# Optimization experiments

Hardware: AMD Instinct MI355X
Metric: run time of the kernel (lower is better)

## Reference

```python
import jax, jax.numpy as jnp
import numpy as np

B, T, D = 64, 512, 512
H, DH = 8, 64  # head_num, att_embedding_size; H*DH == D
NEG = jnp.float32(-2.0**32 + 1)


def _pos_encoding(t, d):
    # Position_Embedding (mode='sum'): [cos, sin] concat over d/2 frequencies
    inv_freq = 1.0 / jnp.power(10000.0, 2.0 * jnp.arange(d // 2, dtype=jnp.float32) / d)
    pij = jnp.arange(t, dtype=jnp.float32)[:, None] * inv_freq[None, :]  # (T, d/2)
    return jnp.concatenate([jnp.cos(pij), jnp.sin(pij)], axis=-1)  # (T, d)


def setup_inputs() -> dict:
    key = jax.random.key(0)
    ks = jax.random.split(key, 9)
    queries = jax.random.normal(ks[0], (B, T, D), dtype=jnp.float32)
    keys = jax.random.normal(ks[1], (B, T, D), dtype=jnp.float32)
    query_lens = jax.random.randint(ks[2], (B, 1), 1, T + 1)
    key_lens = jax.random.randint(ks[3], (B, 1), 1, T + 1)
    W_Q = jax.random.truncated_normal(ks[4], -2., 2., (D, H * DH), dtype=jnp.float32) * 0.05
    W_K = jax.random.truncated_normal(ks[5], -2., 2., (D, H * DH), dtype=jnp.float32) * 0.05
    W_V = jax.random.truncated_normal(ks[6], -2., 2., (D, H * DH), dtype=jnp.float32) * 0.05
    fw1 = jax.random.normal(ks[7], (H * DH, 4 * H * DH), dtype=jnp.float32) * 0.02
    fw2 = jax.random.normal(ks[8], (4 * H * DH, H * DH), dtype=jnp.float32) * 0.02
    return {"queries": queries, "keys": keys, "query_lens": query_lens,
            "key_lens": key_lens, "W_Q": W_Q, "W_K": W_K, "W_V": W_V,
            "fw1": fw1, "fw2": fw2}


def reference(queries, keys, query_lens, key_lens, W_Q, W_K, W_V, fw1, fw2):
    # sequence masks (B, T) from lengths (B, 1)
    ar = jnp.arange(T)
    q_mask = (ar[None, :] < query_lens).astype(jnp.float32)  # (B, T)
    k_mask = ar[None, :] < key_lens                          # (B, T) bool

    pe = _pos_encoding(T, D)[None]  # (1, T, D)
    q_in = queries + pe
    k_in = keys + pe

    qp = jnp.einsum('btd,de->bte', q_in, W_Q).reshape(B, T, H, DH)
    kp = jnp.einsum('btd,de->bte', k_in, W_K)
    # DeepCTR quirk: values projected from the already-projected keys
    vp = jnp.einsum('btd,de->bte', kp, W_V).reshape(B, T, H, DH)
    kp = kp.reshape(B, T, H, DH)

    scores = jnp.einsum('bthd,bshd->bhts', qp, kp) / jnp.sqrt(jnp.float32(DH))
    scores = jnp.where(k_mask[:, None, None, :], scores, NEG)
    scores = scores - jnp.max(scores, axis=-1, keepdims=True)
    attn = jax.nn.softmax(scores, axis=-1)
    attn = attn * q_mask[:, None, :, None]

    out = jnp.einsum('bhts,bshd->bthd', attn, vp).reshape(B, T, H * DH)
    result = out + q_in  # residual uses PE-augmented queries

    ff = jnp.einsum('btd,df->btf', jax.nn.relu(jnp.einsum('btd,df->btf', result, fw1)), fw2)
    result = result + ff

    return jnp.mean(result, axis=1, keepdims=True)  # (B, 1, D)
```

## Files before the change

### kernel.cpp

```cpp
#include <hip/hip_runtime.h>

typedef unsigned short u16;
typedef __attribute__((ext_vector_type(8))) short short8;
typedef __attribute__((ext_vector_type(4))) float floatx4;

#define QSCALE 0.1803368801111204f

__device__ __forceinline__ u16 f2bf(float x) {
  union { float f; unsigned u; } un; un.f = x;
  unsigned r = un.u + 0x7fffu + ((un.u >> 16) & 1u);
  return (u16)(r >> 16);
}
__device__ __forceinline__ float bf2f(u16 h) {
  union { unsigned u; float f; } un; un.u = ((unsigned)h) << 16;
  return un.f;
}
__device__ __forceinline__ void gld16(const u16* g, u16* l) {
  __builtin_amdgcn_global_load_lds((__attribute__((address_space(1))) void*)g,
                                   (__attribute__((address_space(3))) void*)l, 16, 0, 0);
}

__global__ __launch_bounds__(256) void wtrans_all(const float* __restrict__ W_Q,
                                                  const float* __restrict__ W_K,
                                                  const float* __restrict__ fw1,
                                                  u16* __restrict__ WqT, u16* __restrict__ WkT,
                                                  u16* __restrict__ F1T) {
  __shared__ float tile[32][33];
  int L = blockIdx.x;
  const float* in;
  u16* out;
  int N, bx, by;
  if (L < 256) { in = W_Q; out = WqT; N = 512; bx = L & 15; by = L >> 4; }
  else if (L < 512) { L -= 256; in = W_K; out = WkT; N = 512; bx = L & 15; by = L >> 4; }
  else { L -= 512; in = fw1; out = F1T; N = 2048; bx = L & 63; by = L >> 6; }
  int tx = threadIdx.x, ty = threadIdx.y;
  int n0 = bx * 32, k0 = by * 32;
#pragma unroll
  for (int i = 0; i < 4; i++) {
    int kk = ty + i * 8;
    tile[kk][tx] = in[(size_t)(k0 + kk) * N + n0 + tx];
  }
  __syncthreads();
#pragma unroll
  for (int i = 0; i < 4; i++) {
    int nn = ty + i * 8;
    out[(size_t)(n0 + nn) * 512 + k0 + tx] = f2bf(tile[tx][nn]);
  }
}

__global__ __launch_bounds__(256) void wkv_kernel(const float* __restrict__ WK,
                                                  const float* __restrict__ WV,
                                                  u16* __restrict__ WkvT) {
  __shared__ float Kt[32][36];
  __shared__ float Vt[32][36];
  int nt = blockIdx.x & 15, dt = blockIdx.x >> 4;
  int n0 = nt * 32, d0 = dt * 32;
  int tid = threadIdx.x;
  int flat = tid * 4;
  int i4 = flat >> 5, j4 = flat & 31;
  int tn = tid & 15, td = tid >> 4;
  float acc00 = 0.f, acc01 = 0.f, acc10 = 0.f, acc11 = 0.f;
  for (int e0 = 0; e0 < 512; e0 += 32) {
    __syncthreads();
    *(float4*)&Kt[i4][j4] = *(const float4*)&WK[(size_t)(d0 + i4) * 512 + e0 + j4];
    *(float4*)&Vt[i4][j4] = *(const float4*)&WV[(size_t)(e0 + i4) * 512 + n0 + j4];
    __syncthreads();
#pragma unroll 8
    for (int e = 0; e < 32; e++) {
      float k0v = Kt[td * 2][e], k1v = Kt[td * 2 + 1][e];
      float v0 = Vt[e][tn * 2], v1 = Vt[e][tn * 2 + 1];
      acc00 += k0v * v0; acc01 += k0v * v1;
      acc10 += k1v * v0; acc11 += k1v * v1;
    }
  }
  size_t o = (size_t)(n0 + tn * 2) * 512 + d0 + td * 2;
  WkvT[o] = f2bf(acc00);
  WkvT[o + 1] = f2bf(acc10);
  WkvT[o + 512] = f2bf(acc01);
  WkvT[o + 513] = f2bf(acc11);
}

__global__ __launch_bounds__(256) void pe_add_kernel(const float* __restrict__ q,
                                                     const float* __restrict__ k,
                                                     u16* __restrict__ qb, u16* __restrict__ kb) {
  size_t flat = ((size_t)blockIdx.x * 256 + threadIdx.x) * 4;
  int d0 = (int)(flat & 511);
  int t = (int)((flat >> 9) & 511);
  const float4 qv = *(const float4*)(q + flat);
  const float4 kv = *(const float4*)(k + flat);
  float pe[4];
#pragma unroll
  for (int i = 0; i < 4; i++) {
    int d = d0 + i;
    int j = (d < 256) ? d : d - 256;
    float f = exp2f((float)j * -0.05190512648f);
    float arg = (float)t * f;
    pe[i] = (d < 256) ? cosf(arg) : sinf(arg);
  }
  u16 qo[4], ko[4];
  qo[0] = f2bf(qv.x + pe[0]); qo[1] = f2bf(qv.y + pe[1]);
  qo[2] = f2bf(qv.z + pe[2]); qo[3] = f2bf(qv.w + pe[3]);
  ko[0] = f2bf(kv.x + pe[0]); ko[1] = f2bf(kv.y + pe[1]);
  ko[2] = f2bf(kv.z + pe[2]); ko[3] = f2bf(kv.w + pe[3]);
  *(uint2*)(qb + flat) = *(const uint2*)qo;
  *(uint2*)(kb + flat) = *(const uint2*)ko;
}

template <int EPI, int MODE>
__global__ __launch_bounds__(256) void gemm_bt(const u16* __restrict__ A, const u16* __restrict__ Bt,
                                               u16* __restrict__ C, int NX, int KS, int N, int K,
                                               float* __restrict__ outp,
                                               const u16* __restrict__ A2, const u16* __restrict__ Bt2,
                                               u16* __restrict__ C2,
                                               const u16* __restrict__ A3, const u16* __restrict__ Bt3,
                                               u16* __restrict__ C3) {
  __shared__ u16 pool[16640];
  u16* Alds = pool;
  u16* Blds = pool + 8192;
  const int tid = threadIdx.x;
  const int lane = tid & 63, w = tid >> 6;
  const int quad = lane >> 4, cl = lane & 15;
  const int wm = w >> 1, wn = w & 1;
  int L = blockIdx.x;
  int seg = 0;
  if (MODE == 2) {
    int third = gridDim.x / 3;
    seg = L / third;
    L -= seg * third;
    if (seg == 1) { A = A2; Bt = Bt2; C = C2; }
    else if (seg == 2) { A = A3; Bt = Bt3; C = C3; }
  }
  const int xcd = L & 7, s = L >> 3;
  const int nx = s % NX;
  const int t2 = s / NX;
  const int ksl = t2 % KS;
  const int rgrp = t2 / KS;
  const int tm = (rgrp * 8 + xcd) * 128;
  const int tn = nx * 128;
  const int kbase = ksl * (K / KS);
  floatx4 acc[4][4] = {};
  const int nk = (K / KS) >> 6;
  const int srow = lane >> 3;
  const int sg = (lane & 7) ^ srow;
  for (int ks = 0; ks < nk; ks++) {
    __syncthreads();
    const int k0 = kbase + (ks << 6);
#pragma unroll
    for (int i = 0; i < 4; i++) {
      int c = w * 4 + i;
      int row = c * 8 + srow;
      gld16(A + ((size_t)(tm + row) * K + k0 + sg * 8), &Alds[c * 512]);
      gld16(Bt + ((size_t)(tn + row) * K + k0 + sg * 8), &Blds[c * 512]);
    }
    __syncthreads();
#pragma unroll
    for (int kh = 0; kh < 2; kh++) {
      short8 af[4], bfr[4];
      const int ga = (((kh << 2) + quad) ^ (cl & 7)) * 8;
#pragma unroll
      for (int f = 0; f < 4; f++) {
        af[f] = *(const short8*)&Alds[(wm * 64 + f * 16 + cl) * 64 + ga];
        bfr[f] = *(const short8*)&Blds[(wn * 64 + f * 16 + cl) * 64 + ga];
      }
#pragma unroll
      for (int fm = 0; fm < 4; fm++)
#pragma unroll
        for (int fn = 0; fn < 4; fn++)
          acc[fm][fn] = __builtin_amdgcn_mfma_f32_16x16x32_bf16(af[fm], bfr[fn], acc[fm][fn], 0, 0, 0);
    }
  }
  if constexpr (MODE == 2) {
    if (seg < 2) {
#pragma unroll
      for (int fm = 0; fm < 4; fm++)
#pragma unroll
        for (int fn = 0; fn < 4; fn++)
#pragma unroll
          for (int r = 0; r < 4; r++) {
            int row = tm + wm * 64 + fm * 16 + quad * 4 + r;
            int col = tn + wn * 64 + fn * 16 + cl;
            C[(size_t)row * N + col] = f2bf(acc[fm][fn][r]);
          }
    } else {
      __syncthreads();
      u16* Tr = pool;
#pragma unroll
      for (int fm = 0; fm < 4; fm++)
#pragma unroll
        for (int fn = 0; fn < 4; fn++)
#pragma unroll
          for (int r = 0; r < 4; r++) {
            int row = wm * 64 + fm * 16 + quad * 4 + r;
            int col = wn * 64 + fn * 16 + cl;
            Tr[col * 130 + row] = f2bf(acc[fm][fn][r]);
          }
      __syncthreads();
      int col = tid >> 1, half = tid & 1;
      int b = tm >> 9, gcol = tn + col;
      int h = gcol >> 6, d = gcol & 63;
      int s0 = (tm & 511) + half * 64;
      u16* dst = C + ((size_t)((b * 8 + h) * 64 + d) * 512 + s0);
      const u16* src = &Tr[col * 130 + half * 64];
#pragma unroll
      for (int j = 0; j < 8; j++) *(short8*)(dst + j * 8) = *(const short8*)(src + j * 8);
    }
  } else if constexpr (EPI == 0) {
#pragma unroll
    for (int fm = 0; fm < 4; fm++)
#pragma unroll
      for (int fn = 0; fn < 4; fn++)
#pragma unroll
        for (int r = 0; r < 4; r++) {
          int row = tm + wm * 64 + fm * 16 + quad * 4 + r;
          int col = tn + wn * 64 + fn * 16 + cl;
          C[(size_t)row * N + col] = f2bf(acc[fm][fn][r]);
        }
  } else if constexpr (EPI == 2) {
    __shared__ float red[256];
    float csum[4] = {0.f, 0.f, 0.f, 0.f};
#pragma unroll
    for (int fm = 0; fm < 4; fm++)
#pragma unroll
      for (int fn = 0; fn < 4; fn++)
#pragma unroll
        for (int r = 0; r < 4; r++) csum[fn] += fmaxf(acc[fm][fn][r], 0.0f);
#pragma unroll
    for (int fn = 0; fn < 4; fn++) {
      csum[fn] += __shfl_xor(csum[fn], 16);
      csum[fn] += __shfl_xor(csum[fn], 32);
    }
    __syncthreads();
    if (quad == 0) {
#pragma unroll
      for (int fn = 0; fn < 4; fn++) red[wm * 128 + wn * 64 + fn * 16 + cl] = csum[fn];
    }
    __syncthreads();
    if (tid < 128) {
      int wn2 = tid >> 6, c2 = tid & 63;
      float tot = red[wn2 * 64 + c2] + red[128 + wn2 * 64 + c2];
      int b = tm >> 9;
      atomicAdd(outp + (size_t)b * N + tn + wn2 * 64 + c2, tot);
    }
  }
}

__global__ __launch_bounds__(256) void ffn2_mean_kernel(const float* __restrict__ sums,
                                                        const float* __restrict__ fw2,
                                                        float* __restrict__ outp) {
  __shared__ float s[128];
  int fs = blockIdx.x & 15, b = blockIdx.x >> 4;
  int tid = threadIdx.x;
  if (tid < 128) s[tid] = sums[(size_t)b * 2048 + fs * 128 + tid];
  __syncthreads();
  const float* w = fw2 + (size_t)(fs * 128) * 512;
  float a0 = 0.f, a1 = 0.f;
#pragma unroll 4
  for (int f = 0; f < 128; f++) {
    float sv = s[f];
    a0 += sv * w[(size_t)f * 512 + tid];
    a1 += sv * w[(size_t)f * 512 + 256 + tid];
  }
  atomicAdd(outp + b * 512 + tid, a0 * (1.0f / 512.0f));
  atomicAdd(outp + b * 512 + 256 + tid, a1 * (1.0f / 512.0f));
}

__global__ __launch_bounds__(256) void attn_kernel(const u16* __restrict__ qp, const u16* __restrict__ kp,
                                                   const u16* __restrict__ vT, const u16* __restrict__ qin,
                                                   u16* __restrict__ resout, const int* __restrict__ qlen,
                                                   const int* __restrict__ klen, float* __restrict__ outp) {
  __shared__ u16 KPu[8704];
  __shared__ u16 Vlds[64 * 128];
  __shared__ float Csum[4][64];
  int L = blockIdx.x;
  int xcd = L & 7;
  int idx = L >> 3;
  int qt = idx & 7;
  int g = xcd + (idx >> 3) * 8;
  int h = g & 7, b = g >> 3;
  int tid = threadIdx.x, lane = tid & 63, w = tid >> 6;
  int quad = lane >> 4, cl = lane & 15;
  int kl = klen[b], ql = qlen[b];
  int q0 = qt * 64 + w * 16;

  if (qt * 64 >= ql) {
    int c = tid & 63, r0 = (tid >> 6) * 16;
    float sv = 0.f;
#pragma unroll
    for (int i = 0; i < 16; i++) {
      size_t idx2 = ((size_t)(b * 512 + qt * 64 + r0 + i) * 512) + h * 64 + c;
      u16 val = qin[idx2];
      resout[idx2] = val;
      sv += bf2f(val);
    }
    Csum[w][c] = sv;
    __syncthreads();
    if (tid < 64) {
      float t = Csum[0][tid] + Csum[1][tid] + Csum[2][tid] + Csum[3][tid];
      atomicAdd(outp + b * 512 + h * 64 + tid, t * (1.0f / 512.0f));
    }
    return;
  }
  bool wactive = q0 < ql;

  short8 qfrag[2];
#pragma unroll
  for (int ks = 0; ks < 2; ks++)
    qfrag[ks] = *(const short8*)(qp + ((size_t)(b * 512 + q0 + cl) * 512 + h * 64 + ks * 32 + quad * 8));
  const short8 ones8 = {(short)0x3F80, (short)0x3F80, (short)0x3F80, (short)0x3F80,
                        (short)0x3F80, (short)0x3F80, (short)0x3F80, (short)0x3F80};
  float m_r[4];
  floatx4 o[4] = {};
  floatx4 lacc = {};
#pragma unroll
  for (int r = 0; r < 4; r++) m_r[r] = -3.0e38f;

  int nkt = (kl + 127) >> 7;
  for (int kt = 0; kt < nkt; kt++) {
    __syncthreads();
#pragma unroll
    for (int i = 0; i < 4; i++) {
      int c = w * 4 + i;
      int row = c * 8 + (lane >> 3);
      int gc = (lane & 7) ^ (row & 7);
      gld16(kp + ((size_t)(b * 512 + kt * 128 + row) * 512 + h * 64 + gc * 8), &KPu[c * 512]);
    }
#pragma unroll
    for (int i = 0; i < 4; i++) {
      int c = w * 4 + i;
      int row = c * 4 + (lane >> 4);
      int gc = (lane & 15) ^ (row & 7);
      gld16(vT + ((size_t)((b * 8 + h) * 64 + row) * 512 + kt * 128 + gc * 8), &Vlds[c * 512]);
    }
    asm volatile("s_waitcnt vmcnt(4)" ::: "memory");
    __builtin_amdgcn_s_barrier();
    __builtin_amdgcn_sched_barrier(0);
    floatx4 sacc[8] = {};
    float mnew[4], alpha[4];
    if (wactive) {
      __builtin_amdgcn_s_setprio(1);
#pragma unroll
      for (int f = 0; f < 8; f++) {
        int krow = f * 16 + cl;
#pragma unroll
        for (int ks = 0; ks < 2; ks++) {
          int kc = ks * 4 + quad;
          short8 kf = *(const short8*)&KPu[krow * 64 + ((kc ^ (cl & 7)) * 8)];
          sacc[f] = __builtin_amdgcn_mfma_f32_16x16x32_bf16(qfrag[ks], kf, sacc[f], 0, 0, 0);
        }
      }
      __builtin_amdgcn_s_setprio(0);
#pragma unroll
      for (int r = 0; r < 4; r++) mnew[r] = m_r[r];
#pragma unroll
      for (int f = 0; f < 8; f++) {
        int key = kt * 128 + f * 16 + cl;
        bool ok = key < kl;
#pragma unroll
        for (int r = 0; r < 4; r++) {
          float v = ok ? sacc[f][r] * QSCALE : -4294967296.0f;
          sacc[f][r] = v;
          mnew[r] = fmaxf(mnew[r], v);
        }
      }
#pragma unroll
      for (int mk = 1; mk <= 8; mk <<= 1)
#pragma unroll
        for (int r = 0; r < 4; r++) mnew[r] = fmaxf(mnew[r], __shfl_xor(mnew[r], mk));
#pragma unroll
      for (int r = 0; r < 4; r++) {
        alpha[r] = exp2f(m_r[r] - mnew[r]);
        m_r[r] = mnew[r];
      }
    }
    __syncthreads();
    if (wactive) {
      u16* P = &KPu[w * 2176];
#pragma unroll
      for (int f = 0; f < 8; f++)
#pragma unroll
        for (int r = 0; r < 4; r++) {
          float p = exp2f(sacc[f][r] - mnew[r]);
          P[(quad * 4 + r) * 136 + f * 16 + cl] = f2bf(p);
        }
#pragma unroll
      for (int r = 0; r < 4; r++) lacc[r] *= alpha[r];
#pragma unroll
      for (int fd = 0; fd < 4; fd++)
#pragma unroll
        for (int r = 0; r < 4; r++) o[fd][r] *= alpha[r];
      __builtin_amdgcn_s_setprio(1);
#pragma unroll
      for (int k2 = 0; k2 < 4; k2++) {
        short8 pf = *(const short8*)&P[cl * 136 + k2 * 32 + quad * 8];
        lacc = __builtin_amdgcn_mfma_f32_16x16x32_bf16(pf, ones8, lacc, 0, 0, 0);
#pragma unroll
        for (int fd = 0; fd < 4; fd++) {
          int vrow = fd * 16 + cl;
          int sc = k2 * 4 + quad;
          short8 vf = *(const short8*)&Vlds[vrow * 128 + ((sc ^ (cl & 7)) * 8)];
          o[fd] = __builtin_amdgcn_mfma_f32_16x16x32_bf16(pf, vf, o[fd], 0, 0, 0);
        }
      }
      __builtin_amdgcn_s_setprio(0);
    }
  }
  float colsum[4] = {0.f, 0.f, 0.f, 0.f};
#pragma unroll
  for (int fd = 0; fd < 4; fd++)
#pragma unroll
    for (int r = 0; r < 4; r++) {
      int q = q0 + quad * 4 + r;
      float v = o[fd][r] / lacc[r];
      if (q >= ql) v = 0.f;
      size_t idx2 = (size_t)(b * 512 + q) * 512 + h * 64 + fd * 16 + cl;
      v += bf2f(qin[idx2]);
      resout[idx2] = f2bf(v);
      colsum[fd] += v;
    }
#pragma unroll
  for (int fd = 0; fd < 4; fd++) {
    colsum[fd] += __shfl_xor(colsum[fd], 16);
    colsum[fd] += __shfl_xor(colsum[fd], 32);
  }
  if (quad == 0) {
#pragma unroll
    for (int fd = 0; fd < 4; fd++) Csum[w][fd * 16 + cl] = colsum[fd];
  }
  __syncthreads();
  if (tid < 64) {
    float t = Csum[0][tid] + Csum[1][tid] + Csum[2][tid] + Csum[3][tid];
    atomicAdd(outp + b * 512 + h * 64 + tid, t * (1.0f / 512.0f));
  }
}

extern "C" void kernel_launch(void* const* d_in, const int* in_sizes, int n_in,
                              void* d_out, int out_size, void* d_ws, size_t ws_size,
                              hipStream_t stream) {
  const float* queries = (const float*)d_in[0];
  const float* keys = (const float*)d_in[1];
  const int* qlen = (const int*)d_in[2];
  const int* klen = (const int*)d_in[3];
  const float* W_Q = (const float*)d_in[4];
  const float* W_K = (const float*)d_in[5];
  const float* W_V = (const float*)d_in[6];
  const float* fw1 = (const float*)d_in[7];
  const float* fw2 = (const float*)d_in[8];
  float* outp = (float*)d_out;
  char* ws = (char*)d_ws;

  constexpr size_t SZ_W = 512 * 512 * 2;
  constexpr size_t SZ_F = 2048 * 512 * 2;
  constexpr size_t SZ_S = 64 * 2048 * 4;
  constexpr size_t SZ_T = (size_t)64 * 512 * 512 * 2;
  size_t o_WqT = 0;
  size_t o_WkT = o_WqT + SZ_W;
  size_t o_Wkv = o_WkT + SZ_W;
  size_t o_F1T = o_Wkv + SZ_W;
  size_t o_SUM = o_F1T + SZ_F;
  size_t o_ABCD = o_SUM + SZ_S;
  size_t o_E = o_ABCD + 4 * SZ_T;
  size_t NEED = o_E + SZ_T;
  if (ws_size < NEED) return;

  u16* WqT = (u16*)(ws + o_WqT);
  u16* WkT = (u16*)(ws + o_WkT);
  u16* WkvT = (u16*)(ws + o_Wkv);
  u16* F1T = (u16*)(ws + o_F1T);
  float* sums = (float*)(ws + o_SUM);
  u16* q_in = (u16*)(ws + o_ABCD);
  u16* k_in = (u16*)(ws + o_ABCD + SZ_T);
  u16* qp = (u16*)(ws + o_ABCD + 2 * SZ_T);
  u16* kpb = (u16*)(ws + o_ABCD + 3 * SZ_T);
  u16* vT = (u16*)(ws + o_E);
  u16* resb = k_in;

  hipMemsetAsync(d_out, 0, (size_t)out_size * sizeof(float), stream);
  hipMemsetAsync(sums, 0, SZ_S, stream);

  wtrans_all<<<1536, dim3(32, 8), 0, stream>>>(W_Q, W_K, fw1, WqT, WkT, F1T);
  wkv_kernel<<<256, 256, 0, stream>>>(W_K, W_V, WkvT);
  pe_add_kernel<<<16384, 256, 0, stream>>>(queries, keys, q_in, k_in);

  gemm_bt<0, 2><<<3 * 1024, 256, 0, stream>>>(q_in, WqT, qp, 4, 1, 512, 512, nullptr,
                                              k_in, WkT, kpb, k_in, WkvT, vT);

  attn_kernel<<<4096, 256, 0, stream>>>(qp, kpb, vT, q_in, resb, qlen, klen, outp);

  gemm_bt<2, 0><<<16 * 256, 256, 0, stream>>>(resb, F1T, nullptr, 16, 1, 2048, 512, sums,
                                              nullptr, nullptr, nullptr, nullptr, nullptr, nullptr);
  ffn2_mean_kernel<<<1024, 256, 0, stream>>>(sums, fw2, outp);
}
```

Baseline: 421.9 us.

## Replace FFN1 GEMM with dedicated 256x256-tile kernel using 8 waves

Adds a dedicated FFN1 kernel that computes 256x256 output tiles with 512 threads per block. It double-buffers direct global-to-LDS loads with staggered A/B prefetch and raises wave priority around MFMA bursts. It also maps blocks across XCDs so row groups share L2. The fused ReLU column-sum epilogue now does atomics straight from registers without an LDS reduction, which raises the atomic count per tile. The larger tiles cut operand reloads, at the cost of high register pressure and fewer blocks in flight.

```diff
diff --git a/kernel.cpp b/kernel.cpp
--- a/kernel.cpp
+++ b/kernel.cpp
@@ -215,32 +215,154 @@
           int col = tn + wn * 64 + fn * 16 + cl;
           C[(size_t)row * N + col] = f2bf(acc[fm][fn][r]);
         }
-  } else if constexpr (EPI == 2) {
-    __shared__ float red[256];
-    float csum[4] = {0.f, 0.f, 0.f, 0.f};
-#pragma unroll
-    for (int fm = 0; fm < 4; fm++)
-#pragma unroll
-      for (int fn = 0; fn < 4; fn++)
-#pragma unroll
-        for (int r = 0; r < 4; r++) csum[fn] += fmaxf(acc[fm][fn][r], 0.0f);
-#pragma unroll
-    for (int fn = 0; fn < 4; fn++) {
-      csum[fn] += __shfl_xor(csum[fn], 16);
-      csum[fn] += __shfl_xor(csum[fn], 32);
-    }
-    __syncthreads();
-    if (quad == 0) {
-#pragma unroll
-      for (int fn = 0; fn < 4; fn++) red[wm * 128 + wn * 64 + fn * 16 + cl] = csum[fn];
-    }
-    __syncthreads();
-    if (tid < 128) {
-      int wn2 = tid >> 6, c2 = tid & 63;
-      float tot = red[wn2 * 64 + c2] + red[128 + wn2 * 64 + c2];
-      int b = tm >> 9;
-      atomicAdd(outp + (size_t)b * N + tn + wn2 * 64 + c2, tot);
-    }
+  }
+}
+
+__global__ __launch_bounds__(512, 2) void ffn1_256(const u16* __restrict__ A,
+                                                   const u16* __restrict__ Bt,
+                                                   float* __restrict__ outp) {
+  __shared__ u16 lds[65536];
+  const int K = 512;
+  const int tid = threadIdx.x;
+  const int lane = tid & 63, w = tid >> 6;
+  const int quad = lane >> 4, cl = lane & 15;
+  const int wm = w >> 2, wn = w & 3;
+  int L = blockIdx.x;
+  const int xcd = L & 7, s = L >> 3;
+  const int nx = s & 7;
+  const int rgrp = s >> 3;
+  const int tm = (rgrp * 8 + xcd) * 256;
+  const int tn = nx * 256;
+  const int srow = lane >> 3;
+  const int sg = (lane & 7) ^ srow;
+  const int cb = w * 4;
+
+  floatx4 acc[8][4] = {};
+
+  {
+    u16* Ab = lds;
+    u16* Bb = lds + 16384;
+#pragma unroll
+    for (int i = 0; i < 4; i++) {
+      int cc = cb + i, row = cc * 8 + srow;
+      gld16(A + ((size_t)(tm + row) * K + sg * 8), &Ab[cc * 512]);
+    }
+#pragma unroll
+    for (int i = 0; i < 4; i++) {
+      int cc = cb + i, row = cc * 8 + srow;
+      gld16(Bt + ((size_t)(tn + row) * K + sg * 8), &Bb[cc * 512]);
+    }
+  }
+
+  const int nk = K >> 6;
+#pragma unroll 1
+  for (int kt = 0; kt < nk; kt++) {
+    u16* Ab = lds + (kt & 1) * 32768;
+    u16* Bb = Ab + 16384;
+    u16* An = lds + ((kt & 1) ^ 1) * 32768;
+    u16* Bn = An + 16384;
+    const bool pf = (kt + 1 < nk);
+    const int k0n = (kt + 1) << 6;
+    if (pf) {
+#pragma unroll
+      for (int i = 0; i < 4; i++) {
+        int cc = cb + i, row = cc * 8 + srow;
+        gld16(A + ((size_t)(tm + row) * K + k0n + sg * 8), &An[cc * 512]);
+      }
+      asm volatile("s_waitcnt vmcnt(4)" ::: "memory");
+    } else {
+      asm volatile("s_waitcnt vmcnt(0)" ::: "memory");
+    }
+    __builtin_amdgcn_s_barrier();
+    short8 a0[4][2], b0[2][2];
+#pragma unroll
+    for (int f = 0; f < 4; f++)
+#pragma unroll
+      for (int kh = 0; kh < 2; kh++)
+        a0[f][kh] = *(const short8*)&Ab[(wm * 128 + f * 16 + cl) * 64 + ((((kh << 2) + quad)) ^ (cl & 7)) * 8];
+#pragma unroll
+    for (int n = 0; n < 2; n++)
+#pragma unroll
+      for (int kh = 0; kh < 2; kh++)
+        b0[n][kh] = *(const short8*)&Bb[(wn * 64 + n * 16 + cl) * 64 + ((((kh << 2) + quad)) ^ (cl & 7)) * 8];
+    __builtin_amdgcn_s_setprio(1);
+#pragma unroll
+    for (int f = 0; f < 4; f++)
+#pragma unroll
+      for (int n = 0; n < 2; n++)
+#pragma unroll
+        for (int kh = 0; kh < 2; kh++)
+          acc[f][n] = __builtin_amdgcn_mfma_f32_16x16x32_bf16(a0[f][kh], b0[n][kh], acc[f][n], 0, 0, 0);
+    __builtin_amdgcn_s_setprio(0);
+    __builtin_amdgcn_s_barrier();
+    if (pf) {
+#pragma unroll
+      for (int i = 0; i < 4; i++) {
+        int cc = cb + i, row = cc * 8 + srow;
+        gld16(Bt + ((size_t)(tn + row) * K + k0n + sg * 8), &Bn[cc * 512]);
+      }
+    }
+    short8 b1[2][2];
+#pragma unroll
+    for (int n = 0; n < 2; n++)
+#pragma unroll
+      for (int kh = 0; kh < 2; kh++)
+        b1[n][kh] = *(const short8*)&Bb[(wn * 64 + (n + 2) * 16 + cl) * 64 + ((((kh << 2) + quad)) ^ (cl & 7)) * 8];
+    __builtin_amdgcn_s_setprio(1);
+#pragma unroll
+    for (int f = 0; f < 4; f++)
+#pragma unroll
+      for (int n = 0; n < 2; n++)
+#pragma unroll
+        for (int kh = 0; kh < 2; kh++)
+          acc[f][n + 2] = __builtin_amdgcn_mfma_f32_16x16x32_bf16(a0[f][kh], b1[n][kh], acc[f][n + 2], 0, 0, 0);
+    __builtin_amdgcn_s_setprio(0);
+    __builtin_amdgcn_s_barrier();
+    short8 a1[4][2];
+#pragma unroll
+    for (int f = 0; f < 4; f++)
+#pragma unroll
+      for (int kh = 0; kh < 2; kh++)
+        a1[f][kh] = *(const short8*)&Ab[(wm * 128 + (f + 4) * 16 + cl) * 64 + ((((kh << 2) + quad)) ^ (cl & 7)) * 8];
+    __builtin_amdgcn_s_setprio(1);
+#pragma unroll
+    for (int f = 0; f < 4; f++)
+#pragma unroll
+      for (int n = 0; n < 2; n++)
+#pragma unroll
+        for (int kh = 0; kh < 2; kh++)
+          acc[f + 4][n + 2] = __builtin_amdgcn_mfma_f32_16x16x32_bf16(a1[f][kh], b1[n][kh], acc[f + 4][n + 2], 0, 0, 0);
+    __builtin_amdgcn_s_setprio(0);
+    __builtin_amdgcn_s_barrier();
+    __builtin_amdgcn_s_setprio(1);
+#pragma unroll
+    for (int f = 0; f < 4; f++)
+#pragma unroll
+      for (int n = 0; n < 2; n++)
+#pragma unroll
+        for (int kh = 0; kh < 2; kh++)
+          acc[f + 4][n] = __builtin_amdgcn_mfma_f32_16x16x32_bf16(a1[f][kh], b0[n][kh], acc[f + 4][n], 0, 0, 0);
+    __builtin_amdgcn_s_setprio(0);
+    __builtin_amdgcn_s_barrier();
+  }
+
+  float cs[4] = {0.f, 0.f, 0.f, 0.f};
+#pragma unroll
+  for (int f = 0; f < 8; f++)
+#pragma unroll
+    for (int n = 0; n < 4; n++)
+#pragma unroll
+      for (int r = 0; r < 4; r++) cs[n] += fmaxf(acc[f][n][r], 0.0f);
+#pragma unroll
+  for (int n = 0; n < 4; n++) {
+    cs[n] += __shfl_xor(cs[n], 16);
+    cs[n] += __shfl_xor(cs[n], 32);
+  }
+  if (quad == 0) {
+    int b = tm >> 9;
+#pragma unroll
+    for (int n = 0; n < 4; n++)
+      atomicAdd(outp + (size_t)b * 2048 + tn + wn * 64 + n * 16 + cl, cs[n]);
   }
 }
 
@@ -486,7 +608,6 @@
 
   attn_kernel<<<4096, 256, 0, stream>>>(qp, kpb, vT, q_in, resb, qlen, klen, outp);
 
-  gemm_bt<2, 0><<<16 * 256, 256, 0, stream>>>(resb, F1T, nullptr, 16, 1, 2048, 512, sums,
-                                              nullptr, nullptr, nullptr, nullptr, nullptr, nullptr);
+  ffn1_256<<<1024, 512, 0, stream>>>(resb, F1T, sums);
   ffn2_mean_kernel<<<1024, 256, 0, stream>>>(sums, fw2, outp);
 }
```

After: 404.6 us. 1.04x faster.
